# Optimization experiments

Hardware: AMD Instinct MI355X
Metric: run time of the kernel (lower is better)

## Reference

```python
import jax, jax.numpy as jnp
import numpy as np
from jax import lax


def _binarize(t):
    # sign binarization to +1/-1 (zero maps to -1, matching torch.where(t > 0, 1, -1))
    return jnp.where(t > 0, 1.0, -1.0).astype(t.dtype)


def _bconv(x, w, b):
    # binary conv: binarize input and weights, then standard 3x3 'same' conv
    y = lax.conv_general_dilated(
        _binarize(x), _binarize(w),
        window_strides=(1, 1), padding=((1, 1), (1, 1)),
        dimension_numbers=('NCHW', 'OIHW', 'NCHW'))
    return y + b[None, :, None, None]


def _maxpool2(x):
    return lax.reduce_window(x, -jnp.inf, lax.max, (1, 1, 2, 2), (1, 1, 2, 2), 'VALID')


def setup_inputs() -> dict:
    key = jax.random.key(0)
    ks = jax.random.split(key, 13)
    s = 0.1
    return {
        'x': jax.random.normal(ks[0], (4096, 1, 28, 28), jnp.float32),
        'w1': jax.random.normal(ks[1], (32, 1, 3, 3), jnp.float32) * s,
        'b1': jax.random.normal(ks[2], (32,), jnp.float32) * s,
        'w2': jax.random.normal(ks[3], (64, 32, 3, 3), jnp.float32) * s,
        'b2': jax.random.normal(ks[4], (64,), jnp.float32) * s,
        'w3': jax.random.normal(ks[5], (16, 64, 3, 3), jnp.float32) * s,
        'b3': jax.random.normal(ks[6], (16,), jnp.float32) * s,
        'fc1_w': jax.random.normal(ks[7], (256, 16 * 7 * 7), jnp.float32) * s,
        'fc1_b': jax.random.normal(ks[8], (256,), jnp.float32) * s,
        'fc2_w': jax.random.normal(ks[9], (128, 256), jnp.float32) * s,
        'fc2_b': jax.random.normal(ks[10], (128,), jnp.float32) * s,
        'fc3_w': jax.random.normal(ks[11], (10, 128), jnp.float32) * s,
        'fc3_b': jax.random.normal(ks[12], (10,), jnp.float32) * s,
    }


def reference(x, w1, b1, w2, b2, w3, b3, fc1_w, fc1_b, fc2_w, fc2_b, fc3_w, fc3_b):
    h = jax.nn.relu(_maxpool2(_bconv(x, w1, b1)))      # [B,32,14,14]
    h = jax.nn.relu(_maxpool2(_bconv(h, w2, b2)))      # [B,64,7,7]
    h = jax.nn.relu(_bconv(h, w3, b3))                 # [B,16,7,7]
    h = h.reshape(-1, 16 * 7 * 7)
    h = jax.nn.relu(h @ fc1_w.T + fc1_b)
    h = jax.nn.relu(h @ fc2_w.T + fc2_b)
    return h @ fc3_w.T + fc3_b                          # [B,10]
```

## Files before the change

kernel.cpp:

```cpp
#include <hip/hip_runtime.h>
#include <cstdint>

#define OFF_W1T   4096
#define OFF_W2T   823296
#define OFF_H3T   954368
#define OFF_H1T   14061568
#define OFF_H2T   18255872

#define TW_WB1    0
#define TW_W2     32
#define TW_W3     608
#define TW_CORR2  896
#define TW_CORR3  1920
#define TW_TLE1   2176
#define TW_TGE1   2208
#define TW_TLE2   2240
#define TW_TGE2   2304

__device__ __forceinline__ int imin2(int a, int b) { return a < b ? a : b; }
__device__ __forceinline__ int imax2(int a, int b) { return a > b ? a : b; }

__device__ __forceinline__ void gload16(const float* g, float* lbase, int lane) {
#if __has_builtin(__builtin_amdgcn_global_load_lds)
    __builtin_amdgcn_global_load_lds(
        (const __attribute__((address_space(1))) uint32_t*)g,
        (__attribute__((address_space(3))) uint32_t*)lbase, 16, 0, 0);
#else
    *(float4*)&lbase[lane * 4] = *(const float4*)g;
#endif
}

__global__ __launch_bounds__(256) void prep(
    const float* __restrict__ w1, const float* __restrict__ b1,
    const float* __restrict__ w2, const float* __restrict__ b2,
    const float* __restrict__ w3,
    const float* __restrict__ fc1_w, const float* __restrict__ fc2_w,
    int* __restrict__ tab, float* __restrict__ w1T, float* __restrict__ w2T) {
    int t = threadIdx.x;
    uint32_t* utab = (uint32_t*)tab;
    if (blockIdx.x == 0) {
        if (t < 32) {
            uint32_t b = 0;
            for (int k = 0; k < 9; ++k) b |= (w1[t * 9 + k] > 0.f ? 1u : 0u) << k;
            utab[TW_WB1 + t] = b;
            tab[TW_TLE1 + t] = (int)floorf((9.f + b1[t]) * 0.5f);
            tab[TW_TGE1 + t] = (int)floorf(-b1[t]) + 1;
        }
        if (t >= 32 && t < 96) {
            int oc = t - 32;
            tab[TW_TLE2 + oc] = (int)floorf((288.f + b2[oc]) * 0.5f);
            tab[TW_TGE2 + oc] = (int)floorf(-b2[oc]) + 1;
        }
        for (int idx = t; idx < 576; idx += 256) {
            int oc = idx / 9, tap = idx % 9;
            int kh = tap / 3, kw = tap % 3;
            uint32_t b = 0;
            for (int ic = 0; ic < 32; ++ic)
                b |= (w2[((oc * 32 + ic) * 3 + kh) * 3 + kw] > 0.f ? 1u : 0u) << ic;
            utab[TW_W2 + idx] = b;
        }
        for (int idx = t; idx < 288; idx += 256) {
            int oc = idx / 18, rem = idx % 18;
            int tap = rem >> 1, word = rem & 1;
            int kh = tap / 3, kw = tap % 3;
            uint32_t b = 0;
            for (int ic = 0; ic < 32; ++ic)
                b |= (w3[((oc * 64 + ic + 32 * word) * 3 + kh) * 3 + kw] > 0.f ? 1u : 0u) << ic;
            utab[TW_W3 + idx] = b;
        }
        __syncthreads();
        for (int idx = t; idx < 1024; idx += 256) {
            int pat = idx >> 6, oc = idx & 63;
            int s = 0, n = 0;
            for (int tap = 0; tap < 9; ++tap) {
                int kh = tap / 3, kw = tap % 3;
                bool pad = ((pat & 1) && kh == 0) || ((pat & 2) && kh == 2) ||
                           ((pat & 4) && kw == 0) || ((pat & 8) && kw == 2);
                if (pad) { s += __popc(utab[TW_W2 + oc * 9 + tap]); ++n; }
            }
            tab[TW_CORR2 + idx] = 2 * s - 32 * n;
        }
        if (t < 256) {
            int pat = t >> 4, oc = t & 15;
            int s = 0, n = 0;
            for (int tap = 0; tap < 9; ++tap) {
                int kh = tap / 3, kw = tap % 3;
                bool pad = ((pat & 1) && kh == 0) || ((pat & 2) && kh == 2) ||
                           ((pat & 4) && kw == 0) || ((pat & 8) && kw == 2);
                if (pad) {
                    s += __popc(utab[TW_W3 + oc * 18 + tap * 2]) +
                         __popc(utab[TW_W3 + oc * 18 + tap * 2 + 1]);
                    ++n;
                }
            }
            tab[TW_CORR3 + t] = 2 * s - 64 * n;
        }
    } else if (blockIdx.x <= 52) {
        __shared__ float T[64][65];
        int bb = blockIdx.x - 1;
        int kt = bb >> 2, nt = bb & 3;
#pragma unroll
        for (int s = 0; s < 16; ++s) {
            int idx = s * 256 + t;
            int nl = idx >> 6, kl = idx & 63;
            int k = kt * 64 + kl;
            T[nl][kl] = (k < 784) ? fc1_w[(nt * 64 + nl) * 784 + k] : 0.f;
        }
        __syncthreads();
#pragma unroll
        for (int s = 0; s < 16; ++s) {
            int idx = s * 256 + t;
            int kl = idx >> 6, nl = idx & 63;
            int k = kt * 64 + kl;
            if (k < 800) w1T[k * 256 + nt * 64 + nl] = T[nl][kl];
        }
    } else {
        __shared__ float T[64][65];
        int bb = blockIdx.x - 53;
        int kt = bb >> 1, nt = bb & 1;
#pragma unroll
        for (int s = 0; s < 16; ++s) {
            int idx = s * 256 + t;
            int nl = idx >> 6, kl = idx & 63;
            T[nl][kl] = fc2_w[(nt * 64 + nl) * 256 + kt * 64 + kl];
        }
        __syncthreads();
#pragma unroll
        for (int s = 0; s < 16; ++s) {
            int idx = s * 256 + t;
            int kl = idx >> 6, nl = idx & 63;
            w2T[(kt * 64 + kl) * 128 + nt * 64 + nl] = T[nl][kl];
        }
    }
}

#define WV 456

__global__ __launch_bounds__(512, 8) void conv_stack(
    const float* __restrict__ x,
    const float* __restrict__ b3,
    const int* __restrict__ tab,
    float* __restrict__ h3T) {
    __shared__ int SH[1280 + 4 * WV];
    const int t = threadIdx.x;
    const int wid = t >> 6, lane = t & 63;
    const int iml = wid >> 1, sw = wid & 1;
    const int img = blockIdx.x * 4 + iml;
    const uint32_t* utab = (const uint32_t*)tab;
    uint32_t* W = (uint32_t*)&SH[1280 + iml * WV];

    for (int i = t; i < 1280; i += 512) SH[i] = tab[TW_CORR2 + i];
    for (int i = t; i < 4 * WV; i += 512) SH[1280 + i] = 0;
    __syncthreads();

    if (lane < 14) {
        int r = sw * 14 + lane;
        const float* xr = x + img * 784 + r * 28;
        uint32_t b = 0;
#pragma unroll
        for (int q = 0; q < 7; ++q) {
            float4 v = *(const float4*)(xr + q * 4);
            b |= (v.x > 0.f ? 1u : 0u) << (q * 4 + 0);
            b |= (v.y > 0.f ? 1u : 0u) << (q * 4 + 1);
            b |= (v.z > 0.f ? 1u : 0u) << (q * 4 + 2);
            b |= (v.w > 0.f ? 1u : 0u) << (q * 4 + 3);
        }
        W[1 + r] = b << 1;
    }
    __syncthreads();

    auto conv1_int = [&](int p) {
        int Pi = 1 + p / 12, Pj = 1 + p % 12;
        int i0 = 2 * Pi, j0 = 2 * Pj;
        uint32_t r0 = W[i0], r1 = W[i0 + 1], r2 = W[i0 + 2], r3 = W[i0 + 3];
        uint32_t f0a = (r0 >> j0) & 7, f0b = (r0 >> (j0 + 1)) & 7;
        uint32_t f1a = (r1 >> j0) & 7, f1b = (r1 >> (j0 + 1)) & 7;
        uint32_t f2a = (r2 >> j0) & 7, f2b = (r2 >> (j0 + 1)) & 7;
        uint32_t f3a = (r3 >> j0) & 7, f3b = (r3 >> (j0 + 1)) & 7;
        uint32_t s00 = f0a | (f1a << 3) | (f2a << 6);
        uint32_t s01 = f0b | (f1b << 3) | (f2b << 6);
        uint32_t s10 = f1a | (f2a << 3) | (f3a << 6);
        uint32_t s11 = f1b | (f2b << 3) | (f3b << 6);
        uint32_t word = 0;
#pragma unroll
        for (int oc = 0; oc < 32; ++oc) {
            uint32_t w = utab[TW_WB1 + oc];
            int m0 = __popc(s00 ^ w), m1 = __popc(s01 ^ w);
            int m2 = __popc(s10 ^ w), m3 = __popc(s11 ^ w);
            int mn = imin2(imin2(m0, m1), imin2(m2, m3));
            word |= (mn <= tab[TW_TLE1 + oc] ? 1u : 0u) << oc;
        }
        W[32 + (Pi + 1) * 16 + (Pj + 1)] = word;
    };
    if (sw == 0) {
        conv1_int(lane);
        conv1_int(64 + lane);
    } else {
        if (lane < 16) conv1_int(128 + lane);
        int p = lane;
        bool act = p < 52;
        int pp = act ? p : 28;
        int Pi, Pj;
        if (pp < 14)      { Pi = 0;  Pj = pp; }
        else if (pp < 28) { Pi = 13; Pj = pp - 14; }
        else if (pp < 40) { Pi = pp - 28 + 1; Pj = 0; }
        else              { Pi = pp - 40 + 1; Pj = 13; }
        int i0 = 2 * Pi, j0 = 2 * Pj;
        uint32_t r0 = W[i0], r1 = W[i0 + 1], r2 = W[i0 + 2], r3 = W[i0 + 3];
        uint32_t f0a = (r0 >> j0) & 7, f0b = (r0 >> (j0 + 1)) & 7;
        uint32_t f1a = (r1 >> j0) & 7, f1b = (r1 >> (j0 + 1)) & 7;
        uint32_t f2a = (r2 >> j0) & 7, f2b = (r2 >> (j0 + 1)) & 7;
        uint32_t f3a = (r3 >> j0) & 7, f3b = (r3 >> (j0 + 1)) & 7;
        uint32_t smp[4];
        smp[0] = f0a | (f1a << 3) | (f2a << 6);
        smp[1] = f0b | (f1b << 3) | (f2b << 6);
        smp[2] = f1a | (f2a << 3) | (f3a << 6);
        smp[3] = f1b | (f2b << 3) | (f3b << 6);
        uint32_t mb[4];
        int pcm[4];
#pragma unroll
        for (int a = 0; a < 2; ++a) {
            int i = 2 * Pi + a;
            uint32_t vre = 0x1FF;
            if (i == 0)  vre &= ~0x007u;
            if (i == 27) vre &= ~0x1C0u;
#pragma unroll
            for (int bb = 0; bb < 2; ++bb) {
                int j = 2 * Pj + bb;
                uint32_t vce = 0x1FF;
                if (j == 0)  vce &= ~0x049u;
                if (j == 27) vce &= ~0x124u;
                mb[a * 2 + bb] = vre & vce;
                pcm[a * 2 + bb] = __popc(vre & vce);
            }
        }
        uint32_t word = 0;
#pragma unroll
        for (int oc = 0; oc < 32; ++oc) {
            uint32_t w = utab[TW_WB1 + oc];
            int best = -1000;
#pragma unroll
            for (int p4 = 0; p4 < 4; ++p4) {
                int v = pcm[p4] - 2 * __popc((smp[p4] ^ w) & mb[p4]);
                best = imax2(best, v);
            }
            word |= (best >= tab[TW_TGE1 + oc] ? 1u : 0u) << oc;
        }
        if (act) W[32 + (Pi + 1) * 16 + (Pj + 1)] = word;
    }
    __syncthreads();

    {
        uint32_t w2r[9];
#pragma unroll
        for (int k = 0; k < 9; ++k) w2r[k] = utab[TW_W2 + lane * 9 + k];
        const int tle2 = tab[TW_TLE2 + lane];
        const int tge2 = tab[TW_TGE2 + lane];
        const uint32_t* H1 = W + 32;
        uint32_t* H2 = W + 288;

        for (int q = sw; q < 25; q += 2) {
            int Pi = 1 + q / 5, Pj = 1 + q % 5;
            uint32_t c[16];
#pragma unroll
            for (int r = 0; r < 4; ++r) {
                uint2 lo = *(const uint2*)&H1[(2 * Pi + r) * 16 + 2 * Pj];
                uint2 hi = *(const uint2*)&H1[(2 * Pi + r) * 16 + 2 * Pj + 2];
                c[r * 4 + 0] = lo.x; c[r * 4 + 1] = lo.y;
                c[r * 4 + 2] = hi.x; c[r * 4 + 3] = hi.y;
            }
            int mn = 100000;
#pragma unroll
            for (int a = 0; a < 2; ++a)
#pragma unroll
                for (int bb = 0; bb < 2; ++bb) {
                    int s = 0;
#pragma unroll
                    for (int kh = 0; kh < 3; ++kh)
#pragma unroll
                        for (int kw = 0; kw < 3; ++kw)
                            s += __popc(c[(a + kh) * 4 + (bb + kw)] ^ w2r[kh * 3 + kw]);
                    mn = imin2(mn, s);
                }
            uint64_t bal = __ballot(mn <= tle2);
            if (lane == 0) {
                uint2 wv = make_uint2((uint32_t)bal, (uint32_t)(bal >> 32));
                *(uint2*)&H2[((Pi + 1) * 9 + (Pj + 1)) * 2] = wv;
            }
        }
        for (int bp = sw; bp < 24; bp += 2) {
            int Pi, Pj;
            if (bp < 7)       { Pi = 0; Pj = bp; }
            else if (bp < 14) { Pi = 6; Pj = bp - 7; }
            else if (bp < 19) { Pi = bp - 14 + 1; Pj = 0; }
            else              { Pi = bp - 19 + 1; Pj = 6; }
            uint32_t c[16];
#pragma unroll
            for (int r = 0; r < 4; ++r) {
                uint2 lo = *(const uint2*)&H1[(2 * Pi + r) * 16 + 2 * Pj];
                uint2 hi = *(const uint2*)&H1[(2 * Pi + r) * 16 + 2 * Pj + 2];
                c[r * 4 + 0] = lo.x; c[r * 4 + 1] = lo.y;
                c[r * 4 + 2] = hi.x; c[r * 4 + 3] = hi.y;
            }
            int best = -100000;
#pragma unroll
            for (int a = 0; a < 2; ++a)
#pragma unroll
                for (int bb = 0; bb < 2; ++bb) {
                    int s = 0;
#pragma unroll
                    for (int kh = 0; kh < 3; ++kh)
#pragma unroll
                        for (int kw = 0; kw < 3; ++kw)
                            s += __popc(c[(a + kh) * 4 + (bb + kw)] ^ w2r[kh * 3 + kw]);
                    int i = 2 * Pi + a, j = 2 * Pj + bb;
                    int pat = (i == 0 ? 1 : 0) | (i == 13 ? 2 : 0) |
                              (j == 0 ? 4 : 0) | (j == 13 ? 8 : 0);
                    int D = 288 - 2 * s + SH[pat * 64 + lane];
                    best = imax2(best, D);
                }
            uint64_t bal = __ballot(best >= tge2);
            if (lane == 0) {
                uint2 wv = make_uint2((uint32_t)bal, (uint32_t)(bal >> 32));
                *(uint2*)&H2[((Pi + 1) * 9 + (Pj + 1)) * 2] = wv;
            }
        }
    }
    __syncthreads();

    {
        const uint32_t* H2 = (const uint32_t*)W + 288;
        int oc = lane & 15, sub = lane >> 4;
        uint32_t w3r[18];
#pragma unroll
        for (int k = 0; k < 18; ++k) w3r[k] = utab[TW_W3 + oc * 18 + k];
        float bias3 = b3[oc];
        const int gbeg = sw ? 6 : 0, gend = sw ? 13 : 6;
        for (int g = gbeg; g < gend; ++g) {
            int pos = g * 4 + sub;
            bool act = pos < 49;
            int pp = act ? pos : 0;
            int Pi = pp / 7, Pj = pp % 7;
            int s = 0;
#pragma unroll
            for (int kh = 0; kh < 3; ++kh)
#pragma unroll
                for (int kw = 0; kw < 3; ++kw) {
                    uint2 hv = *(const uint2*)&H2[((Pi + kh) * 9 + (Pj + kw)) * 2];
                    s += __popc(hv.x ^ w3r[(kh * 3 + kw) * 2]) +
                         __popc(hv.y ^ w3r[(kh * 3 + kw) * 2 + 1]);
                }
            int pat = (Pi == 0 ? 1 : 0) | (Pi == 6 ? 2 : 0) |
                      (Pj == 0 ? 4 : 0) | (Pj == 6 ? 8 : 0);
            int D = 576 - 2 * s + SH[1024 + pat * 16 + oc];
            float h = (float)D + bias3;
            h = h > 0.f ? h : 0.f;
            if (act) h3T[(oc * 49 + pp) * 4096 + img] = h;
        }
    }
}

__global__ __launch_bounds__(256) void fc1_gemm(
    const float* __restrict__ aT,
    const float* __restrict__ bT,
    const float* __restrict__ bias,
    float* __restrict__ oT) {
    const int KC = 40;
    __shared__ float As[2][KC * 64];
    __shared__ float Bs[2][KC * 32];
    const int t = threadIdx.x;
    const int lane = t & 63, wid = t >> 6;
    const int tx = t & 15, ty = t >> 4;
    const int img0 = blockIdx.x * 64;
    const int n0 = blockIdx.y * 32;
    float acc[4][2] = {{0.f}};

    auto stage = [&](int buf, int kc) {
        for (int s = wid; s < 15; s += 4) {
            if (s < 10) {
                int kk = s * 4 + (lane >> 4);
                int c = (lane & 15) * 4;
                gload16(&aT[(kc + kk) * 4096 + img0 + c], &As[buf][s * 256], lane);
            } else {
                int seg = s - 10;
                int kk = seg * 8 + (lane >> 3);
                int c = (lane & 7) * 4;
                gload16(&bT[(kc + kk) * 256 + n0 + c], &Bs[buf][seg * 256], lane);
            }
        }
    };

    stage(0, 0);
    asm volatile("s_waitcnt vmcnt(0)" ::: "memory");
    __builtin_amdgcn_s_barrier();
    for (int ch = 0; ch < 20; ++ch) {
        int buf = ch & 1;
        if (ch < 19) {
            stage(buf ^ 1, (ch + 1) * KC);
            asm volatile("s_waitcnt vmcnt(3)" ::: "memory");
        } else {
            asm volatile("s_waitcnt vmcnt(0)" ::: "memory");
        }
        __builtin_amdgcn_s_barrier();
        const float* A = As[buf];
        const float* B = Bs[buf];
#pragma unroll 8
        for (int kk = 0; kk < KC; ++kk) {
            float4 a = *(const float4*)&A[kk * 64 + ty * 4];
            float2 b = *(const float2*)&B[kk * 32 + tx * 2];
            acc[0][0] += a.x * b.x; acc[0][1] += a.x * b.y;
            acc[1][0] += a.y * b.x; acc[1][1] += a.y * b.y;
            acc[2][0] += a.z * b.x; acc[2][1] += a.z * b.y;
            acc[3][0] += a.w * b.x; acc[3][1] += a.w * b.y;
        }
        __builtin_amdgcn_s_barrier();
    }
#pragma unroll
    for (int j = 0; j < 2; ++j) {
        int n = n0 + tx * 2 + j;
        float bj = bias[n];
        float4 ov;
        ov.x = acc[0][j] + bj; ov.x = ov.x > 0.f ? ov.x : 0.f;
        ov.y = acc[1][j] + bj; ov.y = ov.y > 0.f ? ov.y : 0.f;
        ov.z = acc[2][j] + bj; ov.z = ov.z > 0.f ? ov.z : 0.f;
        ov.w = acc[3][j] + bj; ov.w = ov.w > 0.f ? ov.w : 0.f;
        *(float4*)&oT[n * 4096 + img0 + ty * 4] = ov;
    }
}

__global__ __launch_bounds__(256) void fc2_gemm(
    const float* __restrict__ aT,
    const float* __restrict__ bT,
    const float* __restrict__ bias,
    float* __restrict__ oT) {
    const int KC = 64;
    __shared__ float As[2][KC * 64];
    __shared__ float Bs[2][KC * 32];
    const int t = threadIdx.x;
    const int lane = t & 63, wid = t >> 6;
    const int tx = t & 15, ty = t >> 4;
    const int img0 = blockIdx.x * 64;
    const int n0 = blockIdx.y * 32;
    float acc[4][2] = {{0.f}};

    auto stage = [&](int buf, int kc) {
        for (int s = wid; s < 24; s += 4) {
            if (s < 16) {
                int kk = s * 4 + (lane >> 4);
                int c = (lane & 15) * 4;
                gload16(&aT[(kc + kk) * 4096 + img0 + c], &As[buf][s * 256], lane);
            } else {
                int seg = s - 16;
                int kk = seg * 8 + (lane >> 3);
                int c = (lane & 7) * 4;
                gload16(&bT[(kc + kk) * 128 + n0 + c], &Bs[buf][seg * 256], lane);
            }
        }
    };

    stage(0, 0);
    asm volatile("s_waitcnt vmcnt(0)" ::: "memory");
    __builtin_amdgcn_s_barrier();
    for (int ch = 0; ch < 4; ++ch) {
        int buf = ch & 1;
        if (ch < 3) {
            stage(buf ^ 1, (ch + 1) * KC);
            asm volatile("s_waitcnt vmcnt(6)" ::: "memory");
        } else {
            asm volatile("s_waitcnt vmcnt(0)" ::: "memory");
        }
        __builtin_amdgcn_s_barrier();
        const float* A = As[buf];
        const float* B = Bs[buf];
#pragma unroll 8
        for (int kk = 0; kk < KC; ++kk) {
            float4 a = *(const float4*)&A[kk * 64 + ty * 4];
            float2 b = *(const float2*)&B[kk * 32 + tx * 2];
            acc[0][0] += a.x * b.x; acc[0][1] += a.x * b.y;
            acc[1][0] += a.y * b.x; acc[1][1] += a.y * b.y;
            acc[2][0] += a.z * b.x; acc[2][1] += a.z * b.y;
            acc[3][0] += a.w * b.x; acc[3][1] += a.w * b.y;
        }
        __builtin_amdgcn_s_barrier();
    }
#pragma unroll
    for (int j = 0; j < 2; ++j) {
        int n = n0 + tx * 2 + j;
        float bj = bias[n];
        float4 ov;
        ov.x = acc[0][j] + bj; ov.x = ov.x > 0.f ? ov.x : 0.f;
        ov.y = acc[1][j] + bj; ov.y = ov.y > 0.f ? ov.y : 0.f;
        ov.z = acc[2][j] + bj; ov.z = ov.z > 0.f ? ov.z : 0.f;
        ov.w = acc[3][j] + bj; ov.w = ov.w > 0.f ? ov.w : 0.f;
        *(float4*)&oT[n * 4096 + img0 + ty * 4] = ov;
    }
}

__global__ __launch_bounds__(256) void fc3_gemm(
    const float* __restrict__ aT,
    const float* __restrict__ w,
    const float* __restrict__ bias,
    float* __restrict__ out) {
    int id = blockIdx.x * 256 + threadIdx.x;
    int n = id >> 12, img = id & 4095;
    const float* wr = w + n * 128;
    float a0 = 0.f, a1 = 0.f, a2 = 0.f, a3 = 0.f;
#pragma unroll 8
    for (int k = 0; k < 128; k += 4) {
        a0 += aT[(k + 0) * 4096 + img] * wr[k + 0];
        a1 += aT[(k + 1) * 4096 + img] * wr[k + 1];
        a2 += aT[(k + 2) * 4096 + img] * wr[k + 2];
        a3 += aT[(k + 3) * 4096 + img] * wr[k + 3];
    }
    out[img * 10 + n] = (a0 + a1) + (a2 + a3) + bias[n];
}

extern "C" void kernel_launch(void* const* d_in, const int* in_sizes, int n_in,
                              void* d_out, int out_size, void* d_ws, size_t ws_size,
                              hipStream_t stream) {
    const float* x     = (const float*)d_in[0];
    const float* w1    = (const float*)d_in[1];
    const float* b1    = (const float*)d_in[2];
    const float* w2    = (const float*)d_in[3];
    const float* b2    = (const float*)d_in[4];
    const float* w3    = (const float*)d_in[5];
    const float* b3    = (const float*)d_in[6];
    const float* fc1_w = (const float*)d_in[7];
    const float* fc1_b = (const float*)d_in[8];
    const float* fc2_w = (const float*)d_in[9];
    const float* fc2_b = (const float*)d_in[10];
    const float* fc3_w = (const float*)d_in[11];
    const float* fc3_b = (const float*)d_in[12];
    float* out = (float*)d_out;

    const int B = in_sizes[0] / 784;
    char* ws = (char*)d_ws;
    float* w1T = (float*)(ws + OFF_W1T);
    float* w2T = (float*)(ws + OFF_W2T);
    float* h3T = (float*)(ws + OFF_H3T);
    float* h1T = (float*)(ws + OFF_H1T);
    float* h2T = (float*)(ws + OFF_H2T);
    int* tab = (int*)(ws + OFF_H2T);

    hipLaunchKernelGGL(prep, dim3(61), dim3(256), 0, stream,
                       w1, b1, w2, b2, w3, fc1_w, fc2_w, tab, w1T, w2T);
    hipLaunchKernelGGL(conv_stack, dim3(B / 4), dim3(512), 0, stream,
                       x, b3, tab, h3T);
    hipLaunchKernelGGL(fc1_gemm, dim3(B / 64, 8), dim3(256), 0, stream,
                       h3T, w1T, fc1_b, h1T);
    hipLaunchKernelGGL(fc2_gemm, dim3(B / 64, 4), dim3(256), 0, stream,
                       h1T, w2T, fc2_b, h2T);
    hipLaunchKernelGGL(fc3_gemm, dim3(B * 10 / 256), dim3(256), 0, stream,
                       h2T, fc3_w, fc3_b, out);
}
```

Baseline: 215.4 us.

## Read FC weights directly from global memory and widen fc1 tile to 64 outputs

The fc1 and fc2 GEMMs no longer stage the weight matrix through LDS. Each thread now loads its B values straight from global memory, where they are cached across threads. fc1 also doubles its output tile per block from 32 to 64 columns, with a 4x4 register accumulator per thread, which halves the grid's y dimension and the number of times the activation matrix is re-read. This removes LDS traffic and async-copy bookkeeping for weights, but adds global/L1 load latency inside the inner loop and more registers per thread.

```diff
diff --git a/kernel.cpp b/kernel.cpp
--- a/kernel.cpp
+++ b/kernel.cpp
@@ -367,64 +367,61 @@
     float* __restrict__ oT) {
     const int KC = 40;
     __shared__ float As[2][KC * 64];
-    __shared__ float Bs[2][KC * 32];
     const int t = threadIdx.x;
     const int lane = t & 63, wid = t >> 6;
     const int tx = t & 15, ty = t >> 4;
     const int img0 = blockIdx.x * 64;
-    const int n0 = blockIdx.y * 32;
-    float acc[4][2] = {{0.f}};
-
-    auto stage = [&](int buf, int kc) {
-        for (int s = wid; s < 15; s += 4) {
-            if (s < 10) {
-                int kk = s * 4 + (lane >> 4);
-                int c = (lane & 15) * 4;
-                gload16(&aT[(kc + kk) * 4096 + img0 + c], &As[buf][s * 256], lane);
-            } else {
-                int seg = s - 10;
-                int kk = seg * 8 + (lane >> 3);
-                int c = (lane & 7) * 4;
-                gload16(&bT[(kc + kk) * 256 + n0 + c], &Bs[buf][seg * 256], lane);
-            }
+    const int n0 = blockIdx.y * 64;
+    const float* __restrict__ Bp = bT + n0 + tx * 4;
+    float acc[4][4] = {{0.f}};
+
+    auto stageA = [&](int buf, int kc) {
+        for (int s = wid; s < 10; s += 4) {
+            int kk = s * 4 + (lane >> 4);
+            int c = (lane & 15) * 4;
+            gload16(&aT[(kc + kk) * 4096 + img0 + c], &As[buf][s * 256], lane);
         }
     };
 
-    stage(0, 0);
+    stageA(0, 0);
     asm volatile("s_waitcnt vmcnt(0)" ::: "memory");
     __builtin_amdgcn_s_barrier();
     for (int ch = 0; ch < 20; ++ch) {
         int buf = ch & 1;
         if (ch < 19) {
-            stage(buf ^ 1, (ch + 1) * KC);
-            asm volatile("s_waitcnt vmcnt(3)" ::: "memory");
+            stageA(buf ^ 1, (ch + 1) * KC);
+            asm volatile("s_waitcnt vmcnt(2)" ::: "memory");
         } else {
             asm volatile("s_waitcnt vmcnt(0)" ::: "memory");
         }
         __builtin_amdgcn_s_barrier();
         const float* A = As[buf];
-        const float* B = Bs[buf];
+        const float* __restrict__ Bk = Bp + ch * KC * 256;
 #pragma unroll 8
         for (int kk = 0; kk < KC; ++kk) {
             float4 a = *(const float4*)&A[kk * 64 + ty * 4];
-            float2 b = *(const float2*)&B[kk * 32 + tx * 2];
+            float4 b = *(const float4*)&Bk[kk * 256];
             acc[0][0] += a.x * b.x; acc[0][1] += a.x * b.y;
+            acc[0][2] += a.x * b.z; acc[0][3] += a.x * b.w;
             acc[1][0] += a.y * b.x; acc[1][1] += a.y * b.y;
+            acc[1][2] += a.y * b.z; acc[1][3] += a.y * b.w;
             acc[2][0] += a.z * b.x; acc[2][1] += a.z * b.y;
+            acc[2][2] += a.z * b.z; acc[2][3] += a.z * b.w;
             acc[3][0] += a.w * b.x; acc[3][1] += a.w * b.y;
+            acc[3][2] += a.w * b.z; acc[3][3] += a.w * b.w;
         }
         __builtin_amdgcn_s_barrier();
     }
-#pragma unroll
-    for (int j = 0; j < 2; ++j) {
-        int n = n0 + tx * 2 + j;
-        float bj = bias[n];
+    float4 bb = *(const float4*)&bias[n0 + tx * 4];
+    float bv[4] = {bb.x, bb.y, bb.z, bb.w};
+#pragma unroll
+    for (int jj = 0; jj < 4; ++jj) {
         float4 ov;
-        ov.x = acc[0][j] + bj; ov.x = ov.x > 0.f ? ov.x : 0.f;
-        ov.y = acc[1][j] + bj; ov.y = ov.y > 0.f ? ov.y : 0.f;
-        ov.z = acc[2][j] + bj; ov.z = ov.z > 0.f ? ov.z : 0.f;
-        ov.w = acc[3][j] + bj; ov.w = ov.w > 0.f ? ov.w : 0.f;
-        *(float4*)&oT[n * 4096 + img0 + ty * 4] = ov;
+        ov.x = acc[0][jj] + bv[jj]; ov.x = ov.x > 0.f ? ov.x : 0.f;
+        ov.y = acc[1][jj] + bv[jj]; ov.y = ov.y > 0.f ? ov.y : 0.f;
+        ov.z = acc[2][jj] + bv[jj]; ov.z = ov.z > 0.f ? ov.z : 0.f;
+        ov.w = acc[3][jj] + bv[jj]; ov.w = ov.w > 0.f ? ov.w : 0.f;
+        *(float4*)&oT[(n0 + tx * 4 + jj) * 4096 + img0 + ty * 4] = ov;
     }
 }
 
@@ -435,47 +432,40 @@
     float* __restrict__ oT) {
     const int KC = 64;
     __shared__ float As[2][KC * 64];
-    __shared__ float Bs[2][KC * 32];
     const int t = threadIdx.x;
     const int lane = t & 63, wid = t >> 6;
     const int tx = t & 15, ty = t >> 4;
     const int img0 = blockIdx.x * 64;
     const int n0 = blockIdx.y * 32;
+    const float* __restrict__ Bp = bT + n0 + tx * 2;
     float acc[4][2] = {{0.f}};
 
-    auto stage = [&](int buf, int kc) {
-        for (int s = wid; s < 24; s += 4) {
-            if (s < 16) {
-                int kk = s * 4 + (lane >> 4);
-                int c = (lane & 15) * 4;
-                gload16(&aT[(kc + kk) * 4096 + img0 + c], &As[buf][s * 256], lane);
-            } else {
-                int seg = s - 16;
-                int kk = seg * 8 + (lane >> 3);
-                int c = (lane & 7) * 4;
-                gload16(&bT[(kc + kk) * 128 + n0 + c], &Bs[buf][seg * 256], lane);
-            }
+    auto stageA = [&](int buf, int kc) {
+        for (int s = wid; s < 16; s += 4) {
+            int kk = s * 4 + (lane >> 4);
+            int c = (lane & 15) * 4;
+            gload16(&aT[(kc + kk) * 4096 + img0 + c], &As[buf][s * 256], lane);
         }
     };
 
-    stage(0, 0);
+    stageA(0, 0);
     asm volatile("s_waitcnt vmcnt(0)" ::: "memory");
     __builtin_amdgcn_s_barrier();
     for (int ch = 0; ch < 4; ++ch) {
         int buf = ch & 1;
         if (ch < 3) {
-            stage(buf ^ 1, (ch + 1) * KC);
-            asm volatile("s_waitcnt vmcnt(6)" ::: "memory");
+            stageA(buf ^ 1, (ch + 1) * KC);
+            asm volatile("s_waitcnt vmcnt(4)" ::: "memory");
         } else {
             asm volatile("s_waitcnt vmcnt(0)" ::: "memory");
         }
         __builtin_amdgcn_s_barrier();
         const float* A = As[buf];
-        const float* B = Bs[buf];
+        const float* __restrict__ Bk = Bp + ch * KC * 128;
 #pragma unroll 8
         for (int kk = 0; kk < KC; ++kk) {
             float4 a = *(const float4*)&A[kk * 64 + ty * 4];
-            float2 b = *(const float2*)&B[kk * 32 + tx * 2];
+            float2 b = *(const float2*)&Bk[kk * 128];
             acc[0][0] += a.x * b.x; acc[0][1] += a.x * b.y;
             acc[1][0] += a.y * b.x; acc[1][1] += a.y * b.y;
             acc[2][0] += a.z * b.x; acc[2][1] += a.z * b.y;
@@ -546,7 +536,7 @@
                        w1, b1, w2, b2, w3, fc1_w, fc2_w, tab, w1T, w2T);
     hipLaunchKernelGGL(conv_stack, dim3(B / 4), dim3(512), 0, stream,
                        x, b3, tab, h3T);
-    hipLaunchKernelGGL(fc1_gemm, dim3(B / 64, 8), dim3(256), 0, stream,
+    hipLaunchKernelGGL(fc1_gemm, dim3(B / 64, 4), dim3(256), 0, stream,
                        h3T, w1T, fc1_b, h1T);
     hipLaunchKernelGGL(fc2_gemm, dim3(B / 64, 4), dim3(256), 0, stream,
                        h1T, w2T, fc2_b, h2T);
```

Measured after the change: 257.0 us. 19.3% more time.
